# Kernel tuning notes

Hardware: AMD Instinct MI355X
Metric: run time of the kernel (lower is better)

Reference implementation:

```python
import jax, jax.numpy as jnp
import numpy as np

N_LAYER = 2


def setup_inputs() -> dict:
    key = jax.random.key(0)
    k1, k2 = jax.random.split(key)
    seq_len, batch, hidden = 2048, 32, 512
    x = jax.random.normal(k1, (seq_len, batch, hidden), dtype=jnp.float32)
    # torch init: uniform(0, 1) on recurrent weights
    w_hh = jax.random.uniform(k2, (N_LAYER, hidden), dtype=jnp.float32)
    h0 = jnp.zeros((N_LAYER, batch, hidden), dtype=jnp.float32)
    return {"x": x, "w_hh": w_hh, "h0": h0}


def reference(x, w_hh, h0):
    # x: [T, B, H]; w_hh: [L, H]; h0: [L, B, H]
    out = x
    for i in range(N_LAYER):
        w = w_hh[i]  # [H]

        def step(h, xt):
            h_new = jax.nn.relu(xt + h * w)
            return h_new, h_new

        _, out = jax.lax.scan(step, h0[i], out)  # out: [T, B, H]
    return out
```

## Files before the change

kernel.cpp:

```cpp
#include <hip/hip_runtime.h>


#define TSTEPS  2048
#define BATCH   32
#define HID     512
#define BH      (BATCH * HID)
#define PHASE_T 32
#define NPHASE  (TSTEPS / PHASE_T)
#define NSLOT   8
#define SLOT_FLOATS (PHASE_T * 64)
#define SLOT_BYTES  (SLOT_FLOATS * 4)
#define LPP     (PHASE_T / 4)
#define NPROD   4

typedef __attribute__((address_space(1))) const void* gas_cvp;
typedef __attribute__((address_space(3))) void*       las_vp;

#define ISSUE(q)                                                              \
  do {                                                                        \
    char* lb_ = (char*)lds + ((q) & (NSLOT - 1)) * SLOT_BYTES;                \
    const float* gq_ = gp + (size_t)(q) * PHASE_T * BH;                       \
    _Pragma("unroll")                                                         \
    for (int m_ = 0; m_ < LPP; ++m_) {                                        \
      __builtin_amdgcn_global_load_lds((gas_cvp)(gq_ + (size_t)m_ * 4 * BH),  \
                                       (las_vp)(lb_ + m_ * 1024), 16, 0, 0);  \
    }                                                                         \
  } while (0)

__global__ __launch_bounds__(320, 1) void indrnn_mp_kernel(
    const float* __restrict__ x,
    const float* __restrict__ w_hh,
    const float* __restrict__ h0,
    float* __restrict__ out) {
  __shared__ float lds[NSLOT * SLOT_FLOATS];

  const int tid   = threadIdx.x;
  const int wave  = tid >> 6;
  const int lane  = tid & 63;
  const int cbase = blockIdx.x * 64;

  if (wave < NPROD) {
    const int k = wave;
    const int j = lane >> 4;
    const int i = lane & 15;
    const float* gp = x + cbase + (size_t)j * BH + i * 4;

    ISSUE(k);
    ISSUE(k + 4);

    for (int p = 0; p < NPHASE; ++p) {
      if ((p & 3) == k) {
        __builtin_amdgcn_sched_barrier(0);
        if (p + 4 < NPHASE) asm volatile("s_waitcnt vmcnt(8)" ::: "memory");
        else                asm volatile("s_waitcnt vmcnt(0)" ::: "memory");
      }
      __builtin_amdgcn_s_barrier();
      __builtin_amdgcn_sched_barrier(0);
      const int q = p + 7;
      if (q >= 8 && q < NPHASE && (q & 3) == k) ISSUE(q);
    }
  } else {
    const int c   = cbase + lane;
    const int hid = c & (HID - 1);
    const float w1 = w_hh[hid];
    const float w2 = w_hh[HID + hid];
    float h1 = h0[c];
    float h2 = h0[BH + c];
    float* op = out + c;

    for (int p = 0; p < NPHASE; ++p) {
      __builtin_amdgcn_s_barrier();
      __builtin_amdgcn_sched_barrier(0);
      const float* lb = lds + (p & (NSLOT - 1)) * SLOT_FLOATS + lane;
      float* ob = op + (size_t)p * PHASE_T * BH;
#pragma unroll
      for (int u = 0; u < PHASE_T; ++u) {
        const float xv = lb[u * 64];
        h1 = fmaxf(fmaf(w1, h1, xv), 0.0f);
        h2 = fmaxf(fmaf(w2, h2, h1), 0.0f);
        ob[(size_t)u * BH] = h2;
      }
      __builtin_amdgcn_sched_barrier(0);
    }
  }
}

extern "C" void kernel_launch(void* const* d_in, const int* in_sizes, int n_in,
                              void* d_out, int out_size, void* d_ws, size_t ws_size,
                              hipStream_t stream) {
  const float* x    = (const float*)d_in[0];
  const float* w_hh = (const float*)d_in[1];
  const float* h0   = (const float*)d_in[2];
  float* out        = (float*)d_out;

  dim3 grid(BH / 64);
  dim3 block(320);
  hipLaunchKernelGGL(indrnn_mp_kernel, grid, block, 0, stream,
                     x, w_hh, h0, out);
}
```

Measured before the change: 234.1 us.

## Stage outputs in LDS and drain with dedicated store waves

The compute wave now writes its results into an LDS output ring instead of issuing scalar strided global stores. Two new drain waves copy the previous phase's outputs to global memory with float4 stores, so the store traffic overlaps the next phase's recurrence. The four producer waves are reduced to a single loader wave with a 3-deep prefetch into a 4-slot input ring, and the block shrinks to 256 threads. The costs are more LDS traffic, and a single load wave may not issue enough loads to keep up with the memory demand.

Result: no change. 231.9 us (-0.9%).

```diff
diff --git a/kernel.cpp b/kernel.cpp
--- a/kernel.cpp
+++ b/kernel.cpp
@@ -7,18 +7,16 @@
 #define BH      (BATCH * HID)
 #define PHASE_T 32
 #define NPHASE  (TSTEPS / PHASE_T)
-#define NSLOT   8
 #define SLOT_FLOATS (PHASE_T * 64)
 #define SLOT_BYTES  (SLOT_FLOATS * 4)
 #define LPP     (PHASE_T / 4)
-#define NPROD   4
 
 typedef __attribute__((address_space(1))) const void* gas_cvp;
 typedef __attribute__((address_space(3))) void*       las_vp;
 
 #define ISSUE(q)                                                              \
   do {                                                                        \
-    char* lb_ = (char*)lds + ((q) & (NSLOT - 1)) * SLOT_BYTES;                \
+    char* lb_ = (char*)ldsx + ((q) & 3) * SLOT_BYTES;                         \
     const float* gq_ = gp + (size_t)(q) * PHASE_T * BH;                       \
     _Pragma("unroll")                                                         \
     for (int m_ = 0; m_ < LPP; ++m_) {                                        \
@@ -27,61 +25,89 @@
     }                                                                         \
   } while (0)
 
-__global__ __launch_bounds__(320, 1) void indrnn_mp_kernel(
+__global__ __launch_bounds__(256, 1) void indrnn_sw_kernel(
     const float* __restrict__ x,
     const float* __restrict__ w_hh,
     const float* __restrict__ h0,
     float* __restrict__ out) {
-  __shared__ float lds[NSLOT * SLOT_FLOATS];
+  __shared__ float ldsx[4 * SLOT_FLOATS];
+  __shared__ float ldso[4 * SLOT_FLOATS];
 
   const int tid   = threadIdx.x;
   const int wave  = tid >> 6;
   const int lane  = tid & 63;
   const int cbase = blockIdx.x * 64;
 
-  if (wave < NPROD) {
-    const int k = wave;
+  if (wave == 0) {
     const int j = lane >> 4;
     const int i = lane & 15;
     const float* gp = x + cbase + (size_t)j * BH + i * 4;
 
-    ISSUE(k);
-    ISSUE(k + 4);
+    ISSUE(0); ISSUE(1); ISSUE(2);
+    __builtin_amdgcn_sched_barrier(0);
+    asm volatile("s_waitcnt vmcnt(16)" ::: "memory");
 
     for (int p = 0; p < NPHASE; ++p) {
-      if ((p & 3) == k) {
-        __builtin_amdgcn_sched_barrier(0);
-        if (p + 4 < NPHASE) asm volatile("s_waitcnt vmcnt(8)" ::: "memory");
-        else                asm volatile("s_waitcnt vmcnt(0)" ::: "memory");
-      }
       __builtin_amdgcn_s_barrier();
       __builtin_amdgcn_sched_barrier(0);
-      const int q = p + 7;
-      if (q >= 8 && q < NPHASE && (q & 3) == k) ISSUE(q);
+      if (p + 3 < NPHASE) ISSUE(p + 3);
+      __builtin_amdgcn_sched_barrier(0);
+      if (p + 3 < NPHASE)      asm volatile("s_waitcnt vmcnt(16)" ::: "memory");
+      else if (p + 2 < NPHASE) asm volatile("s_waitcnt vmcnt(8)"  ::: "memory");
+      else                     asm volatile("s_waitcnt vmcnt(0)"  ::: "memory");
     }
-  } else {
+    __builtin_amdgcn_s_barrier();
+  } else if (wave == 1) {
     const int c   = cbase + lane;
     const int hid = c & (HID - 1);
     const float w1 = w_hh[hid];
     const float w2 = w_hh[HID + hid];
     float h1 = h0[c];
     float h2 = h0[BH + c];
-    float* op = out + c;
 
     for (int p = 0; p < NPHASE; ++p) {
       __builtin_amdgcn_s_barrier();
       __builtin_amdgcn_sched_barrier(0);
-      const float* lb = lds + (p & (NSLOT - 1)) * SLOT_FLOATS + lane;
-      float* ob = op + (size_t)p * PHASE_T * BH;
+      const float* xb = ldsx + (p & 3) * SLOT_FLOATS + lane;
+      float*       ob = ldso + (p & 3) * SLOT_FLOATS + lane;
 #pragma unroll
       for (int u = 0; u < PHASE_T; ++u) {
-        const float xv = lb[u * 64];
+        const float xv = xb[u * 64];
         h1 = fmaxf(fmaf(w1, h1, xv), 0.0f);
         h2 = fmaxf(fmaf(w2, h2, h1), 0.0f);
-        ob[(size_t)u * BH] = h2;
+        ob[u * 64] = h2;
       }
       __builtin_amdgcn_sched_barrier(0);
+      asm volatile("s_waitcnt lgkmcnt(0)" ::: "memory");
     }
+    __builtin_amdgcn_s_barrier();
+  } else {
+    const int w = wave - 2;
+    const int j = lane >> 4;
+    const int i = lane & 15;
+
+#define DRAIN(q)                                                              \
+    do {                                                                      \
+      const float* sb_ = ldso + ((q) & 3) * SLOT_FLOATS +                     \
+                         (w * 16 + j) * 64 + i * 4;                           \
+      float* gb_ = out + (size_t)((q) * PHASE_T + w * 16 + j) * BH +          \
+                   cbase + i * 4;                                             \
+      _Pragma("unroll")                                                       \
+      for (int m_ = 0; m_ < 4; ++m_) {                                        \
+        const float4 v_ = *(const float4*)(sb_ + m_ * 4 * 64);                \
+        *(float4*)(gb_ + (size_t)m_ * 4 * BH) = v_;                           \
+      }                                                                       \
+    } while (0)
+
+    for (int p = 0; p < NPHASE; ++p) {
+      __builtin_amdgcn_s_barrier();
+      __builtin_amdgcn_sched_barrier(0);
+      if (p >= 1) DRAIN(p - 1);
+    }
+    __builtin_amdgcn_s_barrier();
+    __builtin_amdgcn_sched_barrier(0);
+    DRAIN(NPHASE - 1);
+#undef DRAIN
   }
 }
 
@@ -94,7 +120,7 @@
   float* out        = (float*)d_out;
 
   dim3 grid(BH / 64);
-  dim3 block(320);
-  hipLaunchKernelGGL(indrnn_mp_kernel, grid, block, 0, stream,
+  dim3 block(256);
+  hipLaunchKernelGGL(indrnn_sw_kernel, grid, block, 0, stream,
                      x, w_hh, h0, out);
 }
```
